# Kernel optimization log

Measured on AMD Instinct MI355X. Metric: run time of the kernel, lower is better.

## Reference

```python
import jax, jax.numpy as jnp
import numpy as np

EMBED = 2048
HEADS = 32
HEAD_DIM = 64
MLP_DIM = 8192
TILE = 16
TOP_K = 12
THETA = 500000.0
EPS = 1e-5
NEG = -1e30


def setup_inputs() -> dict:
    key = jax.random.key(0)
    ks = jax.random.split(key, 9)
    B, S = 2, 1024
    w = lambda k, i, o: jax.random.normal(k, (i, o), jnp.float32) * (i ** -0.5)
    return {
        "x": jax.random.normal(ks[0], (B, S, EMBED), jnp.float32),
        "attn_norm_scale": jnp.ones((EMBED,), jnp.float32),
        "wq": w(ks[1], EMBED, HEADS * HEAD_DIM),
        "wk": w(ks[2], EMBED, HEADS * HEAD_DIM),
        "wv": w(ks[3], EMBED, HEADS * HEAD_DIM),
        "wo": w(ks[4], HEADS * HEAD_DIM, EMBED),
        "ffn_norm_scale": jnp.ones((EMBED,), jnp.float32),
        "w_gate": w(ks[5], EMBED, MLP_DIM),
        "w_up": w(ks[6], EMBED, MLP_DIM),
        "w_down": w(ks[7], MLP_DIM, EMBED),
    }


def _rmsnorm(h, g):
    return h * jax.lax.rsqrt(jnp.mean(h * h, axis=-1, keepdims=True) + EPS) * g


def _rope(t, cos, sin):
    # t: [B,S,H,D]; rotate interleaved pairs (llama precompute_freqs_cis style)
    t1, t2 = t[..., 0::2], t[..., 1::2]
    return jnp.stack([t1 * cos - t2 * sin, t1 * sin + t2 * cos], axis=-1).reshape(t.shape)


def reference(x, attn_norm_scale, wq, wk, wv, wo, ffn_norm_scale, w_gate, w_up, w_down):
    B, S, E = x.shape
    n = _rmsnorm(x, attn_norm_scale)
    q = (n @ wq).reshape(B, S, HEADS, HEAD_DIM)
    k = (n @ wk).reshape(B, S, HEADS, HEAD_DIM)
    v = (n @ wv).reshape(B, S, HEADS, HEAD_DIM)

    inv = 1.0 / (THETA ** (jnp.arange(0, HEAD_DIM, 2, dtype=jnp.float32) / HEAD_DIM))
    ang = jnp.arange(S, dtype=jnp.float32)[:, None] * inv  # [S, D/2]
    cos = jnp.cos(ang)[None, :, None, :]
    sin = jnp.sin(ang)[None, :, None, :]
    q = _rope(q, cos, sin)
    k = _rope(k, cos, sin)

    scale = HEAD_DIM ** -0.5
    scores = jnp.einsum("bqhd,bkhd->bhqk", q, k) * scale  # [B,H,S,S]
    causal = jnp.tril(jnp.ones((S, S), dtype=bool))

    # Kascade anchor: per-query top-k key-tile selection on causally-masked scores
    T = S // TILE
    masked = jnp.where(causal, scores, NEG)
    tile_logits = masked.reshape(B, HEADS, S, T, TILE).max(axis=-1)  # [B,H,S,T]
    _, idx = jax.lax.top_k(tile_logits, TOP_K)  # [B,H,S,K]
    sel = jax.nn.one_hot(idx, T, dtype=jnp.float32).sum(axis=-2) > 0  # [B,H,S,T]
    own = jax.nn.one_hot(jnp.arange(S) // TILE, T, dtype=jnp.float32)[None, None] > 0
    key_mask = jnp.repeat(sel | own, TILE, axis=-1)  # [B,H,S,S]
    allowed = key_mask & causal

    probs = jax.nn.softmax(jnp.where(allowed, scores, NEG), axis=-1)
    attn = jnp.einsum("bhqk,bkhd->bqhd", probs, v).reshape(B, S, HEADS * HEAD_DIM)
    x = x + attn @ wo

    n2 = _rmsnorm(x, ffn_norm_scale)
    mlp = (jax.nn.silu(n2 @ w_gate) * (n2 @ w_up)) @ w_down
    return x + mlp
```

## Files before the change

kernel.cpp:

```cpp
#include <hip/hip_runtime.h>
#include <math.h>

typedef __bf16 bf16_t;
typedef bf16_t bf16x8 __attribute__((ext_vector_type(8)));
typedef bf16_t bf16x2 __attribute__((ext_vector_type(2)));
typedef float f32x4 __attribute__((ext_vector_type(4)));

#define EMBED 2048
#define NHEADS 32
#define HDIM 64
#define MLP 8192
#define SEQ 1024
#define NTOK 2048
#define QKV_N 6144

__device__ __forceinline__ void async_copy16(void* lds, const void* g) {
    __builtin_amdgcn_global_load_lds(
        (const __attribute__((address_space(1))) unsigned int*)g,
        (__attribute__((address_space(3))) unsigned int*)lds, 16, 0, 0);
}

template<int CTRL>
__device__ __forceinline__ float dpp_f(float x) {
    return __int_as_float(__builtin_amdgcn_update_dpp(
        __float_as_int(x), __float_as_int(x), CTRL, 0xF, 0xF, false));
}
__device__ __forceinline__ float rowmax16(float v) {
    v = fmaxf(v, dpp_f<0x121>(v));
    v = fmaxf(v, dpp_f<0x122>(v));
    v = fmaxf(v, dpp_f<0x124>(v));
    v = fmaxf(v, dpp_f<0x128>(v));
    return v;
}
__device__ __forceinline__ float rowsum16(float v) {
    v += dpp_f<0x121>(v);
    v += dpp_f<0x122>(v);
    v += dpp_f<0x124>(v);
    v += dpp_f<0x128>(v);
    return v;
}

template<int EPI>
__global__ __launch_bounds__(256) void gemm_bt(
    const bf16_t* __restrict__ A, const bf16_t* __restrict__ Bt,
    void* __restrict__ Cout, const float* __restrict__ Res,
    const bf16_t* __restrict__ Aux,
    int M, int N, int K, int LDK)
{
    __shared__ __align__(16) bf16_t As[128 * 32];
    __shared__ __align__(16) bf16_t Bs[128 * 32];
    const int tid = threadIdx.x;
    const int wave = tid >> 6, lane = tid & 63;
    const int quad = lane >> 4, l15 = lane & 15;
    const int wr = wave >> 1, wc = wave & 1;
    const int m0 = blockIdx.x * 128, n0 = blockIdx.y * 128;
    const int kbeg = blockIdx.z * K;
    const int srow = lane >> 2;
    const int scol = (lane & 3) * 8;

    f32x4 acc[4][4] = {};

    for (int kk = 0; kk < K; kk += 32) {
        const int k0 = kbeg + kk;
        if (kk) __syncthreads();
#pragma unroll
        for (int s = 0; s < 2; ++s) {
            const int chunk = wave * 2 + s;
            const int row = chunk * 16 + srow;
            async_copy16((char*)As + chunk * 1024,
                         A + (size_t)(m0 + row) * LDK + k0 + scol);
            async_copy16((char*)Bs + chunk * 1024,
                         Bt + (size_t)(n0 + row) * LDK + k0 + scol);
        }
        asm volatile("s_waitcnt vmcnt(0)" ::: "memory");
        __syncthreads();

        bf16x8 af[4], bfr[4];
#pragma unroll
        for (int i = 0; i < 4; ++i) {
            af[i]  = *(const bf16x8*)((const char*)As + (wr * 64 + i * 16 + l15) * 64 + quad * 16);
            bfr[i] = *(const bf16x8*)((const char*)Bs + (wc * 64 + i * 16 + l15) * 64 + quad * 16);
        }
#pragma unroll
        for (int i = 0; i < 4; ++i)
#pragma unroll
            for (int j = 0; j < 4; ++j)
                acc[i][j] = __builtin_amdgcn_mfma_f32_16x16x32_bf16(af[i], bfr[j], acc[i][j], 0, 0, 0);
    }

#pragma unroll
    for (int i = 0; i < 4; ++i) {
#pragma unroll
        for (int j = 0; j < 4; ++j) {
#pragma unroll
            for (int r = 0; r < 4; ++r) {
                const int row = m0 + wr * 64 + i * 16 + quad * 4 + r;
                const int col = n0 + wc * 64 + j * 16 + l15;
                const size_t idx = (size_t)row * N + col;
                if (EPI == 0) {
                    ((bf16_t*)Cout)[idx] = (bf16_t)acc[i][j][r];
                } else if (EPI == 1) {
                    ((float*)Cout)[idx] = Res[idx] + acc[i][j][r];
                } else if (EPI == 2) {
                    const float g = (float)Aux[idx];
                    const float s = g / (1.0f + __expf(-g));
                    ((bf16_t*)Cout)[idx] = (bf16_t)(s * acc[i][j][r]);
                } else {
                    unsafeAtomicAdd(&((float*)Cout)[idx], acc[i][j][r]);
                }
            }
        }
    }
}

__global__ __launch_bounds__(256) void copy_f32(
    const float* __restrict__ src, float* __restrict__ dst)
{
    const int i = blockIdx.x * 256 + threadIdx.x;
    ((float4*)dst)[i] = ((const float4*)src)[i];
}

__global__ __launch_bounds__(256) void transpose_cvt(
    const float* __restrict__ src, bf16_t* __restrict__ dst, int K, int N)
{
    __shared__ float tile[32][33];
    const int tx = threadIdx.x & 31, ty = threadIdx.x >> 5;
    const int n0 = blockIdx.x * 32, k0 = blockIdx.y * 32;
#pragma unroll
    for (int i = 0; i < 4; ++i)
        tile[ty + 8 * i][tx] = src[(size_t)(k0 + ty + 8 * i) * N + n0 + tx];
    __syncthreads();
#pragma unroll
    for (int i = 0; i < 4; ++i)
        dst[(size_t)(n0 + ty + 8 * i) * K + k0 + tx] = (bf16_t)tile[tx][ty + 8 * i];
}

__global__ __launch_bounds__(256) void rmsnorm_bf16(
    const float* __restrict__ x, const float* __restrict__ g, bf16_t* __restrict__ out)
{
    const int row = blockIdx.x;
    const int tid = threadIdx.x;
    const float* xr = x + (size_t)row * EMBED + tid * 8;
    const float4 a = *(const float4*)xr;
    const float4 b = *(const float4*)(xr + 4);
    float ss = a.x * a.x + a.y * a.y + a.z * a.z + a.w * a.w
             + b.x * b.x + b.y * b.y + b.z * b.z + b.w * b.w;
#pragma unroll
    for (int off = 1; off < 64; off <<= 1) ss += __shfl_xor(ss, off);
    __shared__ float red[4];
    if ((tid & 63) == 0) red[tid >> 6] = ss;
    __syncthreads();
    const float rs = rsqrtf((red[0] + red[1] + red[2] + red[3]) * (1.0f / EMBED) + 1e-5f);
    const float* gr = g + tid * 8;
    const float xv[8] = {a.x, a.y, a.z, a.w, b.x, b.y, b.z, b.w};
    bf16x8 o;
#pragma unroll
    for (int e = 0; e < 8; ++e) o[e] = (bf16_t)(xv[e] * rs * gr[e]);
    *(bf16x8*)(out + (size_t)row * EMBED + tid * 8) = o;
}

__global__ __launch_bounds__(256) void rope_transpose(
    const bf16_t* __restrict__ qkv, bf16_t* __restrict__ Qh, bf16_t* __restrict__ Kh)
{
    const int id = blockIdx.x * 256 + threadIdx.x;
    const int tok = id >> 5;
    const int h = id & 31;
    const int s = tok & (SEQ - 1);
    const int bh = (tok >> 10) * NHEADS + h;
    const size_t dst = ((size_t)bh * SEQ + s) * HDIM;

    const bf16_t* q = qkv + (size_t)tok * QKV_N + h * HDIM;
    const bf16_t* k = q + EMBED;

    const bf16x2* qp = (const bf16x2*)q;
    const bf16x2* kp = (const bf16x2*)k;
    bf16x2* qo = (bf16x2*)(Qh + dst);
    bf16x2* ko = (bf16x2*)(Kh + dst);
    for (int i = 0; i < 32; ++i) {
        const float inv = exp2f((float)i * -0.59161151779f);
        const float ang = (float)s * inv;
        float sn, cs;
        sincosf(ang, &sn, &cs);
        bf16x2 qv = qp[i], kv = kp[i];
        const float q0 = (float)qv[0], q1 = (float)qv[1];
        const float k0 = (float)kv[0], k1 = (float)kv[1];
        qv[0] = (bf16_t)((q0 * cs - q1 * sn) * 0.125f);
        qv[1] = (bf16_t)((q0 * sn + q1 * cs) * 0.125f);
        kv[0] = (bf16_t)(k0 * cs - k1 * sn);
        kv[1] = (bf16_t)(k0 * sn + k1 * cs);
        qo[i] = qv; ko[i] = kv;
    }
}

__global__ __launch_bounds__(256) void transpose_v(
    const bf16_t* __restrict__ qkv, bf16_t* __restrict__ Vt)
{
    __shared__ bf16_t tile[32][66];
    const int st = blockIdx.x;
    const int bh = blockIdx.y;
    const int b = bh >> 5, h = bh & 31;
    const int tid = threadIdx.x;

    const int d = tid & 63, sr = tid >> 6;
    const bf16_t* src = qkv + (size_t)(b * SEQ + st * 32) * QKV_N + 2 * EMBED + h * HDIM;
#pragma unroll
    for (int i = 0; i < 8; ++i) {
        const int s = i * 4 + sr;
        tile[s][d] = src[(size_t)s * QKV_N + d];
    }
    __syncthreads();
    const int s2 = tid & 31, dr = tid >> 5;
    bf16_t* dstp = Vt + (size_t)bh * HDIM * SEQ + st * 32;
#pragma unroll
    for (int i = 0; i < 8; ++i) {
        const int dd = i * 8 + dr;
        dstp[(size_t)dd * SEQ + s2] = tile[s2][dd];
    }
}

__global__ __launch_bounds__(256, 4) void attn_sparse(
    const bf16_t* __restrict__ Qh, const bf16_t* __restrict__ Kh,
    const bf16_t* __restrict__ Vt, bf16_t* __restrict__ attn)
{
    const int id = blockIdx.x;
    const int xcd = id & 7;
    const int j = id >> 3;
    const int qg = j & 15;
    const int hb = (j >> 4) * 8 + xcd;
    const int h = hb & 31;
    const int b = hb >> 5;
    const int tid  = threadIdx.x;
    const int wave = tid >> 6, lane = tid & 63;
    const int quad = lane >> 4, l15 = lane & 15;
    const int qt = (wave & 1) ? (wave * 16 + 15 - qg) : (wave * 16 + qg);

    __shared__ __align__(16) float  tilemax[4][16][68];
    __shared__ __align__(16) bf16_t Plds[4][16][40];
    __shared__ unsigned long long qmask[4][16];

    const size_t hoff = (size_t)(b * NHEADS + h) * SEQ * HDIM;
    const bf16_t* Qb  = Qh + hoff;
    const bf16_t* Kb  = Kh + hoff;
    const bf16_t* Vtb = Vt + hoff;

    const bf16_t* qrow = Qb + (size_t)(qt * 16 + l15) * HDIM;
    const bf16x8 qf0 = *(const bf16x8*)(qrow + quad * 8);
    const bf16x8 qf1 = *(const bf16x8*)(qrow + 32 + quad * 8);

    const bf16_t* kbase = Kb + (size_t)l15 * HDIM + quad * 8;
    bf16x8 kc0 = *(const bf16x8*)(kbase);
    bf16x8 kc1 = *(const bf16x8*)(kbase + 32);
    for (int t = 0; t <= qt; ++t) {
        const bf16_t* knp = kbase + (size_t)((t < qt) ? t + 1 : t) * (16 * HDIM);
        const bf16x8 kn0 = *(const bf16x8*)(knp);
        const bf16x8 kn1 = *(const bf16x8*)(knp + 32);
        f32x4 sc = {0.f, 0.f, 0.f, 0.f};
        sc = __builtin_amdgcn_mfma_f32_16x16x32_bf16(qf0, kc0, sc, 0, 0, 0);
        sc = __builtin_amdgcn_mfma_f32_16x16x32_bf16(qf1, kc1, sc, 0, 0, 0);
#pragma unroll
        for (int r = 0; r < 4; ++r) {
            const int qr = quad * 4 + r;
            float v = (t == qt && l15 > qr) ? -3.0e38f : sc[r];
            v = rowmax16(v);
            if (l15 == 0) tilemax[wave][qr][t] = v;
        }
        kc0 = kn0; kc1 = kn1;
    }
    asm volatile("s_waitcnt lgkmcnt(0)" ::: "memory");

    if (lane < 16) {
        unsigned long long m = 0;
        const int cnt = qt + 1;
        if (cnt <= 12) {
            m = (1ull << cnt) - 1ull;
        } else {
            const float* tmrow = &tilemax[wave][lane][0];
            const int c4 = qt >> 2;
            for (int it = 0; it < 12; ++it) {
                float best = -3.9e38f; int bi = 0;
                for (int c = 0; c <= c4; ++c) {
                    const float4 v4 = *(const float4*)(tmrow + c * 4);
                    const int tb = c * 4;
                    if (tb + 0 <= qt && !((m >> (tb + 0)) & 1ull) && v4.x > best) { best = v4.x; bi = tb + 0; }
                    if (tb + 1 <= qt && !((m >> (tb + 1)) & 1ull) && v4.y > best) { best = v4.y; bi = tb + 1; }
                    if (tb + 2 <= qt && !((m >> (tb + 2)) & 1ull) && v4.z > best) { best = v4.z; bi = tb + 2; }
                    if (tb + 3 <= qt && !((m >> (tb + 3)) & 1ull) && v4.w > best) { best = v4.w; bi = tb + 3; }
                }
                m |= 1ull << bi;
            }
        }
        m |= 1ull << qt;
        qmask[wave][lane] = m;
    }
    asm volatile("s_waitcnt lgkmcnt(0)" ::: "memory");

    unsigned long long un = 0;
#pragma unroll
    for (int i = 0; i < 16; ++i) un |= qmask[wave][i];
    unsigned long long myrow[4];
#pragma unroll
    for (int r = 0; r < 4; ++r) myrow[r] = qmask[wave][quad * 4 + r];

    float m_run[4], l_run[4];
#pragma unroll
    for (int r = 0; r < 4; ++r) { m_run[r] = -3.0e38f; l_run[r] = 0.f; }
    f32x4 o[4] = {};

    unsigned long long sel = un;
    while (sel) {
        const int t0 = (int)__builtin_ctzll(sel); sel &= sel - 1ull;
        int t1 = -1;
        if (sel) { t1 = (int)__builtin_ctzll(sel); sel &= sel - 1ull; }
        const int t1e = (t1 >= 0) ? t1 : t0;

        const bf16_t* kr0 = Kb + (size_t)(t0 * 16 + l15) * HDIM + quad * 8;
        const bf16x8 k00 = *(const bf16x8*)(kr0);
        const bf16x8 k01 = *(const bf16x8*)(kr0 + 32);
        const bf16_t* kr1 = Kb + (size_t)(t1e * 16 + l15) * HDIM + quad * 8;
        const bf16x8 k10 = *(const bf16x8*)(kr1);
        const bf16x8 k11 = *(const bf16x8*)(kr1 + 32);

        const int colb = ((quad < 2) ? t0 : t1e) * 16 + (quad & 1) * 8;
        bf16x8 vf[4];
#pragma unroll
        for (int jb = 0; jb < 4; ++jb)
            vf[jb] = *(const bf16x8*)(Vtb + (size_t)(jb * 16 + l15) * SEQ + colb);

        f32x4 s0 = {0.f, 0.f, 0.f, 0.f}, s1 = {0.f, 0.f, 0.f, 0.f};
        s0 = __builtin_amdgcn_mfma_f32_16x16x32_bf16(qf0, k00, s0, 0, 0, 0);
        s0 = __builtin_amdgcn_mfma_f32_16x16x32_bf16(qf1, k01, s0, 0, 0, 0);
        s1 = __builtin_amdgcn_mfma_f32_16x16x32_bf16(qf0, k10, s1, 0, 0, 0);
        s1 = __builtin_amdgcn_mfma_f32_16x16x32_bf16(qf1, k11, s1, 0, 0, 0);

#pragma unroll
        for (int r = 0; r < 4; ++r) {
            const int qr = quad * 4 + r;
            const bool ok0 = ((myrow[r] >> t0) & 1ull) && (t0 < qt || l15 <= qr);
            const bool ok1 = (t1 >= 0) && ((myrow[r] >> t1) & 1ull) && (t1 < qt || l15 <= qr);
            const float sv0 = ok0 ? s0[r] : -3.0e38f;
            const float sv1 = ok1 ? s1[r] : -3.0e38f;
            const float mt = rowmax16(fmaxf(sv0, sv1));
            const float mn = fmaxf(m_run[r], mt);
            const float al = __expf(m_run[r] - mn);
            const float p0 = ok0 ? __expf(sv0 - mn) : 0.f;
            const float p1 = ok1 ? __expf(sv1 - mn) : 0.f;
            const float rsum = rowsum16(p0 + p1);
            l_run[r] = l_run[r] * al + rsum;
            m_run[r] = mn;
            Plds[wave][qr][l15]      = (bf16_t)p0;
            Plds[wave][qr][16 + l15] = (bf16_t)p1;
#pragma unroll
            for (int jb = 0; jb < 4; ++jb) o[jb][r] *= al;
        }
        asm volatile("s_waitcnt lgkmcnt(0)" ::: "memory");

        const bf16x8 pa = *(const bf16x8*)&Plds[wave][l15][quad * 8];
#pragma unroll
        for (int jb = 0; jb < 4; ++jb)
            o[jb] = __builtin_amdgcn_mfma_f32_16x16x32_bf16(pa, vf[jb], o[jb], 0, 0, 0);
    }

    const int tok0 = b * SEQ + qt * 16;
#pragma unroll
    for (int r = 0; r < 4; ++r) {
        const int qr = quad * 4 + r;
        const float inv = 1.0f / l_run[r];
        bf16_t* op = attn + (size_t)(tok0 + qr) * EMBED + h * HDIM + l15;
#pragma unroll
        for (int jb = 0; jb < 4; ++jb)
            op[jb * 16] = (bf16_t)(o[jb][r] * inv);
    }
}

extern "C" void kernel_launch(void* const* d_in, const int* in_sizes, int n_in,
                              void* d_out, int out_size, void* d_ws, size_t ws_size,
                              hipStream_t stream)
{
    const float* x   = (const float*)d_in[0];
    const float* ans = (const float*)d_in[1];
    const float* wq  = (const float*)d_in[2];
    const float* wk  = (const float*)d_in[3];
    const float* wv  = (const float*)d_in[4];
    const float* wo  = (const float*)d_in[5];
    const float* fns = (const float*)d_in[6];
    const float* wg  = (const float*)d_in[7];
    const float* wu  = (const float*)d_in[8];
    const float* wd  = (const float*)d_in[9];
    (void)in_sizes; (void)n_in; (void)out_size; (void)ws_size;

    char* ws = (char*)d_ws;
    const size_t MB = 1024 * 1024;
    bf16_t* wt_reg = (bf16_t*)(ws);
    bf16_t* qkv    = (bf16_t*)(ws + 32 * MB);
    bf16_t* attnb  = (bf16_t*)(ws + 56 * MB);
    bf16_t* gate   = (bf16_t*)(ws + 32 * MB);
    float*  x1     = (float* )(ws + 64 * MB);
    bf16_t* nbuf   = (bf16_t*)(ws + 80 * MB);
    bf16_t* Qh     = (bf16_t*)(ws + 88 * MB);
    bf16_t* Kh     = (bf16_t*)(ws + 98 * MB);
    bf16_t* Vt     = (bf16_t*)(ws + 108 * MB);
    bf16_t* hbuf   = (bf16_t*)(ws + 88 * MB);

    transpose_cvt<<<dim3(64, 64), 256, 0, stream>>>(wq, wt_reg,                             EMBED, EMBED);
    transpose_cvt<<<dim3(64, 64), 256, 0, stream>>>(wk, wt_reg + (size_t)EMBED * EMBED,     EMBED, EMBED);
    transpose_cvt<<<dim3(64, 64), 256, 0, stream>>>(wv, wt_reg + (size_t)2 * EMBED * EMBED, EMBED, EMBED);
    rmsnorm_bf16<<<NTOK, 256, 0, stream>>>(x, ans, nbuf);
    gemm_bt<0><<<dim3(16, 48), 256, 0, stream>>>(nbuf, wt_reg, qkv, nullptr, nullptr, NTOK, QKV_N, EMBED, EMBED);
    rope_transpose<<<256, 256, 0, stream>>>(qkv, Qh, Kh);
    transpose_v<<<dim3(32, 64), 256, 0, stream>>>(qkv, Vt);
    attn_sparse<<<1024, 256, 0, stream>>>(Qh, Kh, Vt, attnb);
    transpose_cvt<<<dim3(64, 64), 256, 0, stream>>>(wo, wt_reg, EMBED, EMBED);
    copy_f32<<<4096, 256, 0, stream>>>(x, x1);
    gemm_bt<3><<<dim3(16, 16, 2), 256, 0, stream>>>(attnb, wt_reg, x1, nullptr, nullptr, NTOK, EMBED, EMBED / 2, EMBED);

    rmsnorm_bf16<<<NTOK, 256, 0, stream>>>(x1, fns, nbuf);
    transpose_cvt<<<dim3(256, 64), 256, 0, stream>>>(wg, wt_reg, EMBED, MLP);
    gemm_bt<0><<<dim3(16, 64), 256, 0, stream>>>(nbuf, wt_reg, gate, nullptr, nullptr, NTOK, MLP, EMBED, EMBED);
    transpose_cvt<<<dim3(256, 64), 256, 0, stream>>>(wu, wt_reg, EMBED, MLP);
    gemm_bt<2><<<dim3(16, 64), 256, 0, stream>>>(nbuf, wt_reg, hbuf, nullptr, gate, NTOK, MLP, EMBED, EMBED);
    transpose_cvt<<<dim3(64, 256), 256, 0, stream>>>(wd, wt_reg, MLP, EMBED);
    copy_f32<<<4096, 256, 0, stream>>>(x1, (float*)d_out);
    gemm_bt<3><<<dim3(16, 16, 4), 256, 0, stream>>>(hbuf, wt_reg, (float*)d_out, nullptr, nullptr, NTOK, EMBED, MLP / 4, MLP);
}
```

Measured before the change: 924.4 us.

## Double-buffer GEMM LDS tiles and swizzle block order across XCDs

The bf16 GEMM now keeps two LDS buffers for the A and B tiles. It issues the async global-to-LDS copy for the next K step before running the MFMAs on the current one, so load latency overlaps compute and one barrier per step is dropped. Block indices are also remapped with a stride-8 swizzle so neighbouring tiles land on the same XCD, which should improve L2 reuse. The cost is twice the LDS footprint, which may lower occupancy. The remap hardcodes gridDim.x == 16 and assumes the block count divides by 8.

```diff
diff --git a/kernel.cpp b/kernel.cpp
--- a/kernel.cpp
+++ b/kernel.cpp
@@ -47,45 +47,68 @@
     const bf16_t* __restrict__ Aux,
     int M, int N, int K, int LDK)
 {
-    __shared__ __align__(16) bf16_t As[128 * 32];
-    __shared__ __align__(16) bf16_t Bs[128 * 32];
+    __shared__ __align__(16) bf16_t As[2][128 * 32];
+    __shared__ __align__(16) bf16_t Bs[2][128 * 32];
     const int tid = threadIdx.x;
     const int wave = tid >> 6, lane = tid & 63;
     const int quad = lane >> 4, l15 = lane & 15;
     const int wr = wave >> 1, wc = wave & 1;
-    const int m0 = blockIdx.x * 128, n0 = blockIdx.y * 128;
-    const int kbeg = blockIdx.z * K;
+
+    const int nb  = gridDim.x * gridDim.y * gridDim.z;
+    const int lid = blockIdx.x + gridDim.x * (blockIdx.y + gridDim.y * blockIdx.z);
+    const int sw  = (lid & 7) * (nb >> 3) + (lid >> 3);
+    const int bx  = sw & 15;
+    const int rest = sw >> 4;
+    const int by  = rest % gridDim.y;
+    const int bz  = rest / gridDim.y;
+
+    const int m0 = bx * 128, n0 = by * 128;
     const int srow = lane >> 2;
     const int scol = (lane & 3) * 8;
 
+    const bf16_t* Ap = A  + (size_t)m0 * LDK + (size_t)bz * K;
+    const bf16_t* Bp = Bt + (size_t)n0 * LDK + (size_t)bz * K;
+
     f32x4 acc[4][4] = {};
 
-    for (int kk = 0; kk < K; kk += 32) {
-        const int k0 = kbeg + kk;
-        if (kk) __syncthreads();
+    auto stage = [&](int buf, int kk) {
 #pragma unroll
         for (int s = 0; s < 2; ++s) {
             const int chunk = wave * 2 + s;
             const int row = chunk * 16 + srow;
-            async_copy16((char*)As + chunk * 1024,
-                         A + (size_t)(m0 + row) * LDK + k0 + scol);
-            async_copy16((char*)Bs + chunk * 1024,
-                         Bt + (size_t)(n0 + row) * LDK + k0 + scol);
-        }
-        asm volatile("s_waitcnt vmcnt(0)" ::: "memory");
-        __syncthreads();
+            async_copy16((char*)As[buf] + chunk * 1024,
+                         Ap + (size_t)row * LDK + kk + scol);
+            async_copy16((char*)Bs[buf] + chunk * 1024,
+                         Bp + (size_t)row * LDK + kk + scol);
+        }
+    };
+
+    stage(0, 0);
+    asm volatile("s_waitcnt vmcnt(0)" ::: "memory");
+    __syncthreads();
+
+    const int nsteps = K >> 5;
+    int cur = 0;
+    for (int t = 0; t < nsteps; ++t) {
+        if (t + 1 < nsteps) stage(cur ^ 1, (t + 1) * 32);
 
         bf16x8 af[4], bfr[4];
 #pragma unroll
         for (int i = 0; i < 4; ++i) {
-            af[i]  = *(const bf16x8*)((const char*)As + (wr * 64 + i * 16 + l15) * 64 + quad * 16);
-            bfr[i] = *(const bf16x8*)((const char*)Bs + (wc * 64 + i * 16 + l15) * 64 + quad * 16);
+            af[i]  = *(const bf16x8*)((const char*)As[cur] + (wr * 64 + i * 16 + l15) * 64 + quad * 16);
+            bfr[i] = *(const bf16x8*)((const char*)Bs[cur] + (wc * 64 + i * 16 + l15) * 64 + quad * 16);
         }
 #pragma unroll
         for (int i = 0; i < 4; ++i)
 #pragma unroll
             for (int j = 0; j < 4; ++j)
                 acc[i][j] = __builtin_amdgcn_mfma_f32_16x16x32_bf16(af[i], bfr[j], acc[i][j], 0, 0, 0);
+
+        if (t + 1 < nsteps) {
+            asm volatile("s_waitcnt vmcnt(0)" ::: "memory");
+            __syncthreads();
+        }
+        cur ^= 1;
     }
 
 #pragma unroll
```

Measured after the change: 902.5 us. 2.4% less time.
